# Performance work log

Hardware: AMD Instinct MI355X
Metric: run time of the kernel (lower is better)

Reference implementation:

```python
import jax, jax.numpy as jnp
import numpy as np

B, T, E, H = 64, 512, 256, 128


def setup_inputs() -> dict:
    key = jax.random.key(0)
    ks = jax.random.split(key, 7)
    s = 1.0 / np.sqrt(H)  # PyTorch LSTM default init range
    inputs = jax.random.normal(ks[0], (B, T, E), jnp.float32)
    labels = jax.random.randint(ks[1], (B, T), 0, H)
    W_ih = jax.random.uniform(ks[2], (4 * H, E), jnp.float32, -s, s)
    W_hh = jax.random.uniform(ks[3], (4 * H, H), jnp.float32, -s, s)
    b_ih = jax.random.uniform(ks[4], (4 * H,), jnp.float32, -s, s)
    b_hh = jax.random.uniform(ks[5], (4 * H,), jnp.float32, -s, s)
    transition = jax.random.uniform(ks[6], (H, H), jnp.float32)  # torch.rand
    return {"inputs": inputs, "labels": labels, "W_ih": W_ih, "W_hh": W_hh,
            "b_ih": b_ih, "b_hh": b_hh, "transition": transition}


def _lstm(x, W_ih, W_hh, b_ih, b_hh):
    # x: (T, B, E) -> hs: (T, B, H). PyTorch gate order: i, f, g, o.
    Bn = x.shape[1]
    Hn = W_hh.shape[1]

    def step(carry, xt):
        h, c = carry
        g = xt @ W_ih.T + b_ih + h @ W_hh.T + b_hh  # (B, 4H)
        i, f, gg, o = jnp.split(g, 4, axis=-1)
        c = jax.nn.sigmoid(f) * c + jax.nn.sigmoid(i) * jnp.tanh(gg)
        h = jax.nn.sigmoid(o) * jnp.tanh(c)
        return (h, c), h

    h0 = jnp.zeros((Bn, Hn), x.dtype)
    (_, _), hs = jax.lax.scan(step, (h0, h0), x)
    return hs


def reference(inputs, labels, W_ih, W_hh, b_ih, b_hh, transition):
    x = inputs.transpose(1, 0, 2)  # (T, B, E)
    trans = jax.nn.softmax(transition, axis=1)  # row-softmax transition
    hs = _lstm(x, W_ih, W_hh, b_ih, b_hh)  # (T, B, H)
    Hbth = jax.nn.softmax(hs, axis=2).transpose(1, 0, 2)  # (B, T, H)

    # gold-path score Pr: emissions at gold tags + transition scores
    emit = jnp.take_along_axis(Hbth, labels[:, :, None], axis=2)[..., 0].sum(axis=1)  # (B,)
    tr_score = trans[labels[:, :-1], labels[:, 1:]].sum(axis=1)  # (B,)
    Pr = emit + tr_score

    # CRF forward algorithm (partition score Ps) via scan over time
    pre0 = Hbth[:, 0, :] + trans[0]  # (B, H)

    def crf_step(pre, h_t):
        # Z[b, i, j] = pre[b, i] + trans[i, j] + h_t[b, j]
        Z = pre[:, :, None] + trans[None] + h_t[:, None, :]
        return jax.nn.logsumexp(Z, axis=1), None

    pre, _ = jax.lax.scan(crf_step, pre0, Hbth[:, 1:, :].transpose(1, 0, 2))
    Ps = jax.nn.logsumexp(pre + trans[-1][None, :], axis=1)  # (B,)

    return (Ps - Pr).sum()
```

## Files before the change

kernel.cpp:

```cpp
#include <hip/hip_runtime.h>
#include <hip/hip_bf16.h>
#include <cstdint>

#define BB 64
#define TT 512
#define EE 256
#define HH 128
#define G4 512

typedef _Float16 half2_t __attribute__((ext_vector_type(2)));
typedef _Float16 f16x4 __attribute__((ext_vector_type(4)));
typedef _Float16 f16x8 __attribute__((ext_vector_type(8)));
typedef float f32x4 __attribute__((ext_vector_type(4)));

#define BC(x) __builtin_bit_cast(half2_t, x)

#define BAR() asm volatile("s_waitcnt lgkmcnt(0)\n\ts_barrier" ::: "memory")

__device__ __forceinline__ float fdot2f(half2_t a, half2_t b, float c) {
#if defined(__has_builtin)
#if __has_builtin(__builtin_amdgcn_fdot2)
  return __builtin_amdgcn_fdot2(a, b, c, false);
#else
  return c + (float)a[0] * (float)b[0] + (float)a[1] * (float)b[1];
#endif
#else
  return c + (float)a[0] * (float)b[0] + (float)a[1] * (float)b[1];
#endif
}

__device__ __forceinline__ float rcp_(float x) { return __builtin_amdgcn_rcpf(x); }
__device__ __forceinline__ float sigmoid_(float x) { return rcp_(1.f + __expf(-x)); }
__device__ __forceinline__ float tanh_(float x) {
  float ax = fabsf(x);
  float e = __expf(-2.f * ax);
  float r = (1.f - e) * rcp_(1.f + e);
  return copysignf(r, x);
}

__device__ __forceinline__ float readlane_f(float x, int lane) {
#if defined(__has_builtin)
#if __has_builtin(__builtin_amdgcn_readlane)
  return __builtin_bit_cast(float, __builtin_amdgcn_readlane(__builtin_bit_cast(int, x), lane));
#else
  return __shfl(x, lane);
#endif
#else
  return __shfl(x, lane);
#endif
}

#if defined(__has_builtin)
#if __has_builtin(__builtin_amdgcn_update_dpp)
#define HAVE_DPP 1
#endif
#endif

__device__ __forceinline__ float wave_sum64_bcast(float x) {
#ifdef HAVE_DPP
#define DPP_ADD(ctrl)                                                          \
  {                                                                            \
    int _t = __builtin_amdgcn_update_dpp(0, __builtin_bit_cast(int, x), ctrl,  \
                                         0xf, 0xf, true);                      \
    x += __builtin_bit_cast(float, _t);                                        \
  }
  DPP_ADD(0x111)
  DPP_ADD(0x112)
  DPP_ADD(0x114)
  DPP_ADD(0x118)
  DPP_ADD(0x142)
  DPP_ADD(0x143)
#undef DPP_ADD
  return readlane_f(x, 63);
#else
#pragma unroll
  for (int s = 1; s <= 32; s <<= 1) x += __shfl_xor(x, s);
  return x;
#endif
}

__device__ __host__ __forceinline__ int permj(int j) {
  return ((j & 127) << 2) | (j >> 7);
}

__global__ __launch_bounds__(128) void prep_kernel(
    const float* __restrict__ transition, const float* __restrict__ W_ih,
    float* __restrict__ trans, _Float16* __restrict__ W16) {
  const int bid = blockIdx.x, t = threadIdx.x;
  if (bid < 128) {
    __shared__ float red[2];
    float v = transition[bid * HH + t];
    float m = v;
#pragma unroll
    for (int s = 32; s >= 1; s >>= 1) m = fmaxf(m, __shfl_xor(m, s));
    if ((t & 63) == 0) red[t >> 6] = m;
    __syncthreads();
    m = fmaxf(red[0], red[1]);
    float e = __expf(v - m);
    float s = e;
#pragma unroll
    for (int k = 32; k >= 1; k >>= 1) s += __shfl_xor(s, k);
    __syncthreads();
    if ((t & 63) == 0) red[t >> 6] = s;
    __syncthreads();
    trans[bid * HH + t] = e * rcp_(red[0] + red[1]);
  } else {
    const int base = (bid - 128) * 1024 + t * 8;
    const int row = base >> 8;
    const int col = base & 255;
    float4 v0 = *(const float4*)(W_ih + base);
    float4 v1 = *(const float4*)(W_ih + base + 4);
    f16x8 h;
    h[0] = (_Float16)v0.x; h[1] = (_Float16)v0.y;
    h[2] = (_Float16)v0.z; h[3] = (_Float16)v0.w;
    h[4] = (_Float16)v1.x; h[5] = (_Float16)v1.y;
    h[6] = (_Float16)v1.z; h[7] = (_Float16)v1.w;
    *(f16x8*)(W16 + (size_t)permj(row) * EE + col) = h;
  }
}

__global__ __launch_bounds__(256) void gemm_in(
    const float* __restrict__ A, const _Float16* __restrict__ W16,
    const float* __restrict__ b_ih, const float* __restrict__ b_hh,
    float* __restrict__ out) {
  __shared__ _Float16 As[64][264];
  const int t = threadIdx.x;
  const int m0 = blockIdx.x * 64;
  const int n0 = blockIdx.y * 256;
  {
    const int c4 = t & 63, r0 = t >> 6;
#pragma unroll
    for (int p = 0; p < 16; ++p) {
      const int row = r0 + 4 * p;
      float4 v = *(const float4*)(A + (size_t)(m0 + row) * EE + c4 * 4);
      f16x4 h;
      h[0] = (_Float16)v.x; h[1] = (_Float16)v.y;
      h[2] = (_Float16)v.z; h[3] = (_Float16)v.w;
      *(f16x4*)&As[row][c4 * 4] = h;
    }
  }
  __syncthreads();
  const int w = t >> 6, L = t & 63;
  const int lrow = L & 15, quad = L >> 4, lk = quad * 8;
  f32x4 acc[4][4] = {};
  const _Float16* Wbase = W16 + (size_t)(n0 + w * 64) * EE;
#pragma unroll
  for (int kc = 0; kc < 8; ++kc) {
    f16x8 a[4], bf[4];
#pragma unroll
    for (int mf = 0; mf < 4; ++mf)
      a[mf] = *(const f16x8*)&As[mf * 16 + lrow][kc * 32 + lk];
#pragma unroll
    for (int nf = 0; nf < 4; ++nf)
      bf[nf] = *(const f16x8*)(Wbase + (size_t)(nf * 16 + lrow) * EE + kc * 32 + lk);
#pragma unroll
    for (int mf = 0; mf < 4; ++mf)
#pragma unroll
      for (int nf = 0; nf < 4; ++nf)
        acc[mf][nf] = __builtin_amdgcn_mfma_f32_16x16x32_f16(a[mf], bf[nf], acc[mf][nf], 0, 0, 0);
  }
#pragma unroll
  for (int nf = 0; nf < 4; ++nf) {
    const int j = n0 + w * 64 + nf * 16 + lrow;
    const int jo = ((j & 3) << 7) | (j >> 2);
    const float bias = b_ih[jo] + b_hh[jo];
#pragma unroll
    for (int mf = 0; mf < 4; ++mf) {
#pragma unroll
      for (int r = 0; r < 4; ++r) {
        const int m = m0 + mf * 16 + quad * 4 + r;
        out[(size_t)m * G4 + j] = acc[mf][nf][r] + bias;
      }
    }
  }
}

__global__ __launch_bounds__(512, 1) void lstm_crf(
    const float* __restrict__ precomp, const float* __restrict__ Whh,
    const float* __restrict__ trans, const int* __restrict__ labels,
    float* __restrict__ out_b) {
  const int b = blockIdx.x, t = threadIdx.x;
  const int w = t >> 6, l = t & 63, q = l >> 4, l15 = l & 15;
  const int c2 = l15 & 3;
  const int g2 = t >> 7, jj = t & 127;

  __shared__ __align__(16) _Float16 h_lds[2][HH];
  __shared__ __align__(16) _Float16 E_lds[HH];
  __shared__ __align__(16) float Spart[G4];
  __shared__ int lab[TT];

  f16x8 wfr[4][4];
#pragma unroll
  for (int tf = 0; tf < 4; ++tf) {
    const int rowp = 16 * (4 * w + tf) + l15;
    const int u = rowp >> 2, g = rowp & 3;
    const float* src = Whh + (size_t)(g * HH + u) * HH;
#pragma unroll
    for (int kt = 0; kt < 4; ++kt) {
      const float* s8 = src + kt * 32 + q * 8;
      float4 v0 = *(const float4*)s8;
      float4 v1 = *(const float4*)(s8 + 4);
      f16x8 h8;
      h8[0] = (_Float16)v0.x; h8[1] = (_Float16)v0.y;
      h8[2] = (_Float16)v0.z; h8[3] = (_Float16)v0.w;
      h8[4] = (_Float16)v1.x; h8[5] = (_Float16)v1.y;
      h8[6] = (_Float16)v1.z; h8[7] = (_Float16)v1.w;
      wfr[tf][kt] = h8;
    }
  }
  half2_t et[16];
#pragma unroll
  for (int a = 0; a < 16; ++a) {
    float e0 = __expf(trans[(g2 * 32 + 2 * a) * HH + jj]);
    float e1 = __expf(trans[(g2 * 32 + 2 * a + 1) * HH + jj]);
    half2_t h2; h2[0] = (_Float16)e0; h2[1] = (_Float16)e1;
    et[a] = h2;
  }
  lab[t] = labels[b * TT + t];
  if (t < HH) { h_lds[0][t] = (_Float16)0.f; E_lds[t] = (_Float16)0.f; }

  float tr0x = 0.f, tr0y = 0.f, tr127x = 0.f, tr127y = 0.f;
  if (t < 64) {
    float2 v0 = *(const float2*)(trans + 2 * t);
    float2 v1 = *(const float2*)(trans + 127 * HH + 2 * t);
    tr0x = v0.x; tr0y = v0.y; tr127x = v1.x; tr127y = v1.y;
  }
  float cst = 0.f;
  float preA = 0.f, preB = 0.f, mused = 0.f, emit = 0.f;

  const float* pcb = precomp + (size_t)b * TT * G4 + 64 * w + 4 * q;
  f32x4 pc_cur[4], pc_nxt[4];
#pragma unroll
  for (int tf = 0; tf < 4; ++tf) pc_cur[tf] = *(const f32x4*)(pcb + 16 * tf);
  __syncthreads();

#pragma unroll 1
  for (int step = 0; step < TT; ++step) {
    const int pr = step & 1;
    const int sn = (step < TT - 1) ? step + 1 : step;
#pragma unroll
    for (int tf = 0; tf < 4; ++tf)
      pc_nxt[tf] = *(const f32x4*)(pcb + (size_t)sn * G4 + 16 * tf);
    const f16x8 hb0 = *(const f16x8*)&h_lds[pr][q * 8];
    const f16x8 hb1 = *(const f16x8*)&h_lds[pr][32 + q * 8];
    const f16x8 hb2 = *(const f16x8*)&h_lds[pr][64 + q * 8];
    const f16x8 hb3 = *(const f16x8*)&h_lds[pr][96 + q * 8];
    f32x4 a0 = pc_cur[0], a1 = pc_cur[1], a2 = pc_cur[2], a3 = pc_cur[3];
    a0 = __builtin_amdgcn_mfma_f32_16x16x32_f16(wfr[0][0], hb0, a0, 0, 0, 0);
    a1 = __builtin_amdgcn_mfma_f32_16x16x32_f16(wfr[1][0], hb0, a1, 0, 0, 0);
    a2 = __builtin_amdgcn_mfma_f32_16x16x32_f16(wfr[2][0], hb0, a2, 0, 0, 0);
    a3 = __builtin_amdgcn_mfma_f32_16x16x32_f16(wfr[3][0], hb0, a3, 0, 0, 0);
    a0 = __builtin_amdgcn_mfma_f32_16x16x32_f16(wfr[0][1], hb1, a0, 0, 0, 0);
    a1 = __builtin_amdgcn_mfma_f32_16x16x32_f16(wfr[1][1], hb1, a1, 0, 0, 0);
    a2 = __builtin_amdgcn_mfma_f32_16x16x32_f16(wfr[2][1], hb1, a2, 0, 0, 0);
    a3 = __builtin_amdgcn_mfma_f32_16x16x32_f16(wfr[3][1], hb1, a3, 0, 0, 0);
    a0 = __builtin_amdgcn_mfma_f32_16x16x32_f16(wfr[0][2], hb2, a0, 0, 0, 0);
    a1 = __builtin_amdgcn_mfma_f32_16x16x32_f16(wfr[1][2], hb2, a1, 0, 0, 0);
    a2 = __builtin_amdgcn_mfma_f32_16x16x32_f16(wfr[2][2], hb2, a2, 0, 0, 0);
    a3 = __builtin_amdgcn_mfma_f32_16x16x32_f16(wfr[3][2], hb2, a3, 0, 0, 0);
    a0 = __builtin_amdgcn_mfma_f32_16x16x32_f16(wfr[0][3], hb3, a0, 0, 0, 0);
    a1 = __builtin_amdgcn_mfma_f32_16x16x32_f16(wfr[1][3], hb3, a1, 0, 0, 0);
    a2 = __builtin_amdgcn_mfma_f32_16x16x32_f16(wfr[2][3], hb3, a2, 0, 0, 0);
    a3 = __builtin_amdgcn_mfma_f32_16x16x32_f16(wfr[3][3], hb3, a3, 0, 0, 0);
    float s0 = 0.f, s1 = 0.f;
    const float4* ev4 = (const float4*)E_lds + g2 * 4;
#pragma unroll
    for (int ec = 0; ec < 4; ++ec) {
      float4 eb = ev4[ec];
      s0 = fdot2f(et[4 * ec + 0], BC(eb.x), s0);
      s1 = fdot2f(et[4 * ec + 1], BC(eb.y), s1);
      s0 = fdot2f(et[4 * ec + 2], BC(eb.z), s0);
      s1 = fdot2f(et[4 * ec + 3], BC(eb.w), s1);
    }
    const f32x4 ac = (c2 == 0) ? a0 : (c2 == 1) ? a1 : (c2 == 2) ? a2 : a3;
    const float iv = sigmoid_(ac[0]);
    const float fv = sigmoid_(ac[1]);
    const float gv = tanh_(ac[2]);
    const float ov = sigmoid_(ac[3]);
    cst = fv * cst + iv * gv;
    const float hv = ov * tanh_(cst);
    if (l15 < 4) h_lds[pr ^ 1][16 * w + 4 * l15 + q] = (_Float16)hv;
    Spart[t] = s0 + s1;
    BAR();
    if (t < 64) {
      const half2_t hp = *(const half2_t*)&h_lds[pr ^ 1][2 * t];
      const float h0 = (float)hp[0], h1 = (float)hp[1];
      const float e0 = __expf(h0), e1 = __expf(h1);
      const float denom = wave_sum64_bcast(e0 + e1);
      const float rinv = rcp_(denom);
      const float p0 = e0 * rinv, p1 = e1 * rinv;
      const float2* s2p = (const float2*)Spart;
      float2 Sq0 = s2p[t], Sq1 = s2p[64 + t], Sq2 = s2p[128 + t], Sq3 = s2p[192 + t];
      const float Sa = (Sq0.x + Sq1.x) + (Sq2.x + Sq3.x);
      const float Sb = (Sq0.y + Sq1.y) + (Sq2.y + Sq3.y);
      const float lgSa = __logf(Sa), lgSb = __logf(Sb);
      const float lgS0 = readlane_f(lgSa, 0);
      const int lb = lab[step];
      const float Mnext = (step == 0) ? 0.f : (mused + lgS0);
      preA = p0 + ((step == 0) ? tr0x : (mused + lgSa));
      preB = p1 + ((step == 0) ? tr0y : (mused + lgSb));
      if (2 * t == lb) emit += p0;
      if (2 * t + 1 == lb) emit += p1;
      half2_t Eh;
      Eh[0] = (_Float16)__expf(preA - Mnext);
      Eh[1] = (_Float16)__expf(preB - Mnext);
      *(half2_t*)&E_lds[2 * t] = Eh;
      mused = Mnext;
    }
    BAR();
#pragma unroll
    for (int tf = 0; tf < 4; ++tf) pc_cur[tf] = pc_nxt[tf];
  }
  if (t < 64) {
    float v0 = preA + tr127x, v1 = preB + tr127y;
    float m = fmaxf(v0, v1);
#pragma unroll
    for (int s = 1; s <= 32; s <<= 1) m = fmaxf(m, __shfl_xor(m, s));
    float ex = __expf(v0 - m) + __expf(v1 - m);
    float em = emit;
#pragma unroll
    for (int s = 1; s <= 32; s <<= 1) {
      ex += __shfl_xor(ex, s);
      em += __shfl_xor(em, s);
    }
    if (t == 0) out_b[b] = m + __logf(ex) - em;
  }
}

__global__ __launch_bounds__(512) void finalize_kernel(
    const float* __restrict__ trans, const int* __restrict__ labels,
    const float* __restrict__ out_b, float* __restrict__ d_out) {
  const int t = threadIdx.x;
  float a = 0.f;
  if (t < TT - 1) {
    for (int b = 0; b < BB; ++b) {
      const int l0 = labels[b * TT + t];
      const int l1 = labels[b * TT + t + 1];
      a += trans[l0 * HH + l1];
    }
  }
  float x = ((t < BB) ? out_b[t] : 0.f) - a;
  __shared__ float red[8];
#pragma unroll
  for (int s = 32; s >= 1; s >>= 1) x += __shfl_xor(x, s);
  if ((t & 63) == 0) red[t >> 6] = x;
  __syncthreads();
  if (t == 0) {
    float s = 0.f;
#pragma unroll
    for (int i = 0; i < 8; ++i) s += red[i];
    d_out[0] = s;
  }
}

extern "C" void kernel_launch(void* const* d_in, const int* in_sizes, int n_in,
                              void* d_out, int out_size, void* d_ws, size_t ws_size,
                              hipStream_t stream) {
  const float* inputs = (const float*)d_in[0];
  const int* labels = (const int*)d_in[1];
  const float* W_ih = (const float*)d_in[2];
  const float* W_hh = (const float*)d_in[3];
  const float* b_ih = (const float*)d_in[4];
  const float* b_hh = (const float*)d_in[5];
  const float* transition = (const float*)d_in[6];

  char* ws = (char*)d_ws;
  float* precomp = (float*)ws;
  float* trans = (float*)(ws + 67108864);
  _Float16* W16 = (_Float16*)(ws + 67108864 + 65536);
  float* out_b = (float*)(ws + 67108864 + 65536 + 262144);

  prep_kernel<<<256, 128, 0, stream>>>(transition, W_ih, trans, W16);
  gemm_in<<<dim3(512, 2), 256, 0, stream>>>(inputs, W16, b_ih, b_hh, precomp);
  lstm_crf<<<64, 512, 0, stream>>>(precomp, W_hh, trans, labels, out_b);
  finalize_kernel<<<1, 512, 0, stream>>>(trans, labels, out_b, (float*)d_out);
}
```

Baseline: 579.3 us.

## Spread gate activations across all lanes and move cell update into CRF wave

Each lane now computes one gate activation (sigmoid or tanh through a shared exp/rcp form) instead of every lane computing all four gates redundantly. Activations go to a new shared-memory array, and the first wave then does the cell-state update, h, softmax and CRF step, writing h back to LDS. This cuts per-lane transcendental work on the critical path. In exchange the serial single-wave section gets longer, with extra LDS reads and the tanh(c) computation.

```diff
diff --git a/kernel.cpp b/kernel.cpp
--- a/kernel.cpp
+++ b/kernel.cpp
@@ -181,11 +181,14 @@
     float* __restrict__ out_b) {
   const int b = blockIdx.x, t = threadIdx.x;
   const int w = t >> 6, l = t & 63, q = l >> 4, l15 = l & 15;
-  const int c2 = l15 & 3;
+  const int tf_a = l15 & 3;
+  const int gg = l15 >> 2;
+  const int ua = 16 * w + 4 * tf_a + q;
   const int g2 = t >> 7, jj = t & 127;
 
   __shared__ __align__(16) _Float16 h_lds[2][HH];
   __shared__ __align__(16) _Float16 E_lds[HH];
+  __shared__ __align__(16) float act[G4];
   __shared__ __align__(16) float Spart[G4];
   __shared__ int lab[TT];
 
@@ -225,8 +228,7 @@
     float2 v1 = *(const float2*)(trans + 127 * HH + 2 * t);
     tr0x = v0.x; tr0y = v0.y; tr127x = v1.x; tr127y = v1.y;
   }
-  float cst = 0.f;
-  float preA = 0.f, preB = 0.f, mused = 0.f, emit = 0.f;
+  float c0 = 0.f, c1 = 0.f, preA = 0.f, preB = 0.f, mused = 0.f, emit = 0.f;
 
   const float* pcb = precomp + (size_t)b * TT * G4 + 64 * w + 4 * q;
   f32x4 pc_cur[4], pc_nxt[4];
@@ -272,19 +274,24 @@
       s0 = fdot2f(et[4 * ec + 2], BC(eb.z), s0);
       s1 = fdot2f(et[4 * ec + 3], BC(eb.w), s1);
     }
-    const f32x4 ac = (c2 == 0) ? a0 : (c2 == 1) ? a1 : (c2 == 2) ? a2 : a3;
-    const float iv = sigmoid_(ac[0]);
-    const float fv = sigmoid_(ac[1]);
-    const float gv = tanh_(ac[2]);
-    const float ov = sigmoid_(ac[3]);
-    cst = fv * cst + iv * gv;
-    const float hv = ov * tanh_(cst);
-    if (l15 < 4) h_lds[pr ^ 1][16 * w + 4 * l15 + q] = (_Float16)hv;
+    const f32x4 asel = (tf_a == 0) ? a0 : (tf_a == 1) ? a1 : (tf_a == 2) ? a2 : a3;
+    const float gv = (gg == 0) ? asel[0] : (gg == 1) ? asel[1]
+                   : (gg == 2) ? asel[2] : asel[3];
+    const bool isg = (gg == 2);
+    const float yy = isg ? (-2.f * fabsf(gv)) : (-gv);
+    const float exv = __expf(yy);
+    const float num = isg ? (1.f - exv) : 1.f;
+    float av = num * rcp_(1.f + exv);
+    av = isg ? copysignf(av, gv) : av;
+    act[gg * HH + ua] = av;
     Spart[t] = s0 + s1;
     BAR();
     if (t < 64) {
-      const half2_t hp = *(const half2_t*)&h_lds[pr ^ 1][2 * t];
-      const float h0 = (float)hp[0], h1 = (float)hp[1];
+      const float2* a2p = (const float2*)act;
+      float2 I = a2p[t], F = a2p[64 + t], G = a2p[128 + t], O = a2p[192 + t];
+      c0 = F.x * c0 + I.x * G.x;
+      c1 = F.y * c1 + I.y * G.y;
+      const float h0 = O.x * tanh_(c0), h1 = O.y * tanh_(c1);
       const float e0 = __expf(h0), e1 = __expf(h1);
       const float denom = wave_sum64_bcast(e0 + e1);
       const float rinv = rcp_(denom);
@@ -305,6 +312,9 @@
       Eh[0] = (_Float16)__expf(preA - Mnext);
       Eh[1] = (_Float16)__expf(preB - Mnext);
       *(half2_t*)&E_lds[2 * t] = Eh;
+      half2_t Hh;
+      Hh[0] = (_Float16)h0; Hh[1] = (_Float16)h1;
+      *(half2_t*)&h_lds[pr ^ 1][2 * t] = Hh;
       mused = Mnext;
     }
     BAR();
```

After: 563.1 us. 2.8% less time.
